# Kernel tuning notes

Measured on AMD Instinct MI355X. Metric: run time of the kernel, lower is better.

The kernel has to match this reference:

```python
import jax, jax.numpy as jnp
import numpy as np

L = 3        # num_layers
B = 8192     # batch slots
H = 1024     # hidden_dim (== decoder_in_dim)
D_IN = 1024
D_OUT = 80
N_ACT = 4096 # active rows selected by hidden_idx


def setup_inputs() -> dict:
    key = jax.random.key(0)
    ks = jax.random.split(key, 8)
    encoded = jax.random.normal(ks[0], (B, D_IN), jnp.float32)
    hidden = jax.random.normal(ks[1], (L, B, H), jnp.float32)
    hidden_idx = jnp.arange(N_ACT, dtype=jnp.int32)  # unique, in-range batch indices
    s = 0.05  # small init scale for stable gate math
    w_ih = jax.random.normal(ks[2], (L, 3 * H, D_IN), jnp.float32) * s
    w_hh = jax.random.normal(ks[3], (L, 3 * H, H), jnp.float32) * s
    b_ih = jax.random.normal(ks[4], (L, 3 * H), jnp.float32) * s
    b_hh = jax.random.normal(ks[5], (L, 3 * H), jnp.float32) * s
    w_out = jax.random.normal(ks[6], (D_OUT, H), jnp.float32) * s
    b_out = jax.random.normal(ks[7], (D_OUT,), jnp.float32) * s
    return {"encoded": encoded, "hidden": hidden, "hidden_idx": hidden_idx,
            "w_ih": w_ih, "w_hh": w_hh, "b_ih": b_ih, "b_hh": b_hh,
            "w_out": w_out, "b_out": b_out}


def reference(encoded, hidden, hidden_idx, w_ih, w_hh, b_ih, b_hh, w_out, b_out):
    # Gather active rows, run stacked GRUCells, scatter back (eval mode: dropout = identity).
    x = encoded[hidden_idx]                       # [N, D_IN]
    new_hidden = []
    for i in range(L):                            # small fixed layer loop
        h_full = hidden[i]                        # [B, H]
        h = h_full[hidden_idx]                    # [N, H]
        gi = x @ w_ih[i].T + b_ih[i]              # [N, 3H] gates from input
        gh = h @ w_hh[i].T + b_hh[i]              # [N, 3H] gates from hidden
        i_r, i_z, i_n = jnp.split(gi, 3, axis=-1)
        h_r, h_z, h_n = jnp.split(gh, 3, axis=-1)
        r = jax.nn.sigmoid(i_r + h_r)
        z = jax.nn.sigmoid(i_z + h_z)
        n = jnp.tanh(i_n + r * h_n)
        h_out = (1.0 - z) * n + z * h             # torch GRUCell update
        x = h_out
        new_hidden.append(h_full.at[hidden_idx].set(h_out))
    y = jnp.tanh(x @ w_out.T + b_out)             # linear head + tanh activation
    output = jnp.zeros((B, D_OUT), y.dtype).at[hidden_idx].set(y)
    return (output, jnp.stack(new_hidden))
```

## Files before the change

kernel.cpp:

```cpp
#include <hip/hip_runtime.h>

typedef unsigned short ushort_t;
typedef unsigned int uint_t;
typedef __attribute__((ext_vector_type(8))) short bf16x8;
typedef __attribute__((ext_vector_type(4))) float f32x4;

constexpr int L_   = 3;
constexpr int B_   = 8192;
constexpr int H_   = 1024;
constexpr int DIN_ = 1024;
constexpr int DOUT_= 80;
constexpr int NACT_= 4096;
constexpr int G3_  = 3 * H_;

static __device__ __forceinline__ ushort_t f2bf(float f) {
    uint_t u = __float_as_uint(f);
    uint_t r = (u + 0x7FFFu + ((u >> 16) & 1u)) >> 16;
    return (ushort_t)r;
}

static __device__ __forceinline__ void gll16(const void* g, void* l) {
    __builtin_amdgcn_global_load_lds(
        (const __attribute__((address_space(1))) uint32_t*)g,
        (__attribute__((address_space(3))) uint32_t*)l, 16, 0, 0);
}

__global__ void prep_convert(const float* __restrict__ wih, const float* __restrict__ whh,
                             const float* __restrict__ wout,
                             ushort_t* __restrict__ oih, ushort_t* __restrict__ ohh,
                             ushort_t* __restrict__ oout) {
    int tid = blockIdx.x * blockDim.x + threadIdx.x;
    int nth = gridDim.x * blockDim.x;
    const int NW = L_ * G3_ * H_ / 4;
    for (int i = tid; i < NW; i += nth) {
        float4 a = ((const float4*)wih)[i];
        ushort4 o; o.x = f2bf(a.x); o.y = f2bf(a.y); o.z = f2bf(a.z); o.w = f2bf(a.w);
        ((ushort4*)oih)[i] = o;
        float4 b = ((const float4*)whh)[i];
        ushort4 p; p.x = f2bf(b.x); p.y = f2bf(b.y); p.z = f2bf(b.z); p.w = f2bf(b.w);
        ((ushort4*)ohh)[i] = p;
    }
    const int NO = DOUT_ * H_ / 4;
    for (int i = tid; i < NO; i += nth) {
        float4 a = ((const float4*)wout)[i];
        ushort4 o; o.x = f2bf(a.x); o.y = f2bf(a.y); o.z = f2bf(a.z); o.w = f2bf(a.w);
        ((ushort4*)oout)[i] = o;
    }
}

__global__ void prep_gather(const float* __restrict__ encoded, const float* __restrict__ hidden,
                            const int* __restrict__ idx,
                            ushort_t* __restrict__ x0, ushort_t* __restrict__ hb) {
    const int C4 = H_ / 4;
    const int PER = NACT_ * C4;
    int tid = blockIdx.x * blockDim.x + threadIdx.x;
    int nth = gridDim.x * blockDim.x;
    int total = 4 * PER;
    for (int i = tid; i < total; i += nth) {
        int seg = i / PER;
        int rem = i - seg * PER;
        int r = rem / C4, c = rem % C4;
        int gr = idx[r];
        const float* src = (seg == 0) ? (encoded + (size_t)gr * DIN_)
                                      : (hidden + ((size_t)(seg - 1) * B_ + gr) * H_);
        float4 v = ((const float4*)src)[c];
        ushort4 o; o.x = f2bf(v.x); o.y = f2bf(v.y); o.z = f2bf(v.z); o.w = f2bf(v.w);
        ushort_t* dst = (seg == 0) ? x0 : (hb + (size_t)(seg - 1) * NACT_ * H_);
        ((ushort4*)(dst + (size_t)r * H_))[c] = o;
    }
}

__global__ __launch_bounds__(256, 2) void gru_layer(
    const ushort_t* __restrict__ xb,
    const ushort_t* __restrict__ hb,
    const float* __restrict__ hid_full,
    const ushort_t* __restrict__ wih,
    const ushort_t* __restrict__ whh,
    const float* __restrict__ bih, const float* __restrict__ bhh,
    const int* __restrict__ idx,
    float* __restrict__ out_hid,
    ushort_t* __restrict__ xnext)
{
    __shared__ ushort_t As[128 * 64];
    __shared__ ushort_t Ws[192 * 64];

    const int tid = threadIdx.x;
    const int bid = blockIdx.x;
    const int swz = (bid & 7) * 64 + (bid >> 3);
    const int bn = swz & 15, bm = swz >> 4;
    const int row0 = bm * 128, col0 = bn * 64;
    const int wave = tid >> 6, lane = tid & 63;
    const int wr = wave >> 1, wc = wave & 1;
    const int fl = lane & 15, fh = lane >> 4;
    const int srow = lane >> 3;
    const int sxor = ((lane & 7) ^ srow) * 8;

    f32x4 accR[4][2] = {};
    f32x4 accZ[4][2] = {};
    f32x4 accN[2][4][2] = {};

#pragma unroll
    for (int ph = 0; ph < 2; ++ph) {
        const ushort_t* Asrc = ph ? hb : xb;
        const ushort_t* Wsrc = ph ? whh : wih;
        const ushort_t* abase[4];
        const ushort_t* wbase[6];
#pragma unroll
        for (int t = 0; t < 4; ++t)
            abase[t] = Asrc + (size_t)(row0 + wave * 32 + t * 8 + srow) * H_ + sxor;
#pragma unroll
        for (int t = 0; t < 6; ++t) {
            const int slot = wave * 48 + t * 8 + srow;
            const int gate = slot >> 6, rowW = slot & 63;
            wbase[t] = Wsrc + (size_t)(gate * H_ + col0 + rowW) * H_ + sxor;
        }
        for (int kk = 0; kk < H_; kk += 64) {
            __syncthreads();
#pragma unroll
            for (int t = 0; t < 4; ++t)
                gll16(abase[t] + kk, &As[wave * 2048 + t * 512]);
#pragma unroll
            for (int t = 0; t < 6; ++t)
                gll16(wbase[t] + kk, &Ws[wave * 3072 + t * 512]);
            __syncthreads();
#pragma unroll
            for (int ks = 0; ks < 2; ++ks) {
                const int sl = ((ks * 4 + fh) ^ (fl & 7)) * 8;
                bf16x8 a[4];
#pragma unroll
                for (int m = 0; m < 4; ++m)
                    a[m] = *(const bf16x8*)&As[(wr * 64 + m * 16 + fl) * 64 + sl];
#pragma unroll
                for (int g = 0; g < 3; ++g) {
#pragma unroll
                    for (int n = 0; n < 2; ++n) {
                        const bf16x8 b = *(const bf16x8*)&Ws[(g * 64 + wc * 32 + n * 16 + fl) * 64 + sl];
#pragma unroll
                        for (int m = 0; m < 4; ++m) {
                            if (g == 0)
                                accR[m][n] = __builtin_amdgcn_mfma_f32_16x16x32_bf16(a[m], b, accR[m][n], 0, 0, 0);
                            else if (g == 1)
                                accZ[m][n] = __builtin_amdgcn_mfma_f32_16x16x32_bf16(a[m], b, accZ[m][n], 0, 0, 0);
                            else
                                accN[ph][m][n] = __builtin_amdgcn_mfma_f32_16x16x32_bf16(a[m], b, accN[ph][m][n], 0, 0, 0);
                        }
                    }
                }
            }
        }
    }

#pragma unroll
    for (int m = 0; m < 4; ++m) {
#pragma unroll
        for (int n = 0; n < 2; ++n) {
            const int c = col0 + wc * 32 + n * 16 + fl;
            const float br_r = bih[c] + bhh[c];
            const float br_z = bih[H_ + c] + bhh[H_ + c];
            const float bi_n = bih[2 * H_ + c];
            const float bh_n = bhh[2 * H_ + c];
#pragma unroll
            for (int j = 0; j < 4; ++j) {
                const int r = row0 + wr * 64 + m * 16 + fh * 4 + j;
                const float vr = 1.f / (1.f + expf(-(accR[m][n][j] + br_r)));
                const float vz = 1.f / (1.f + expf(-(accZ[m][n][j] + br_z)));
                const float vn = tanhf(accN[0][m][n][j] + bi_n + vr * (accN[1][m][n][j] + bh_n));
                const int gr = idx[r];
                const float h0 = hid_full[(size_t)gr * H_ + c];
                const float ho = (1.f - vz) * vn + vz * h0;
                out_hid[(size_t)gr * H_ + c] = ho;
                xnext[(size_t)r * H_ + c] = f2bf(ho);
            }
        }
    }
}

__global__ __launch_bounds__(256) void head_gemm(
    const ushort_t* __restrict__ xb, const ushort_t* __restrict__ wo,
    const float* __restrict__ bo, const int* __restrict__ idx,
    float* __restrict__ outy)
{
    __shared__ ushort_t Xs[64][72];
    __shared__ ushort_t Ws[80][72];
    const int tid = threadIdx.x;
    const int row0 = blockIdx.x * 64;
    const int lrow = tid >> 2, lseg = tid & 3;
    const int wave = tid >> 6, lane = tid & 63;
    const int fl = lane & 15, fh = lane >> 4;
    f32x4 acc[5] = {};

    for (int kk = 0; kk < H_; kk += 64) {
        __syncthreads();
        const ushort_t* xp = xb + (size_t)(row0 + lrow) * H_ + kk + lseg * 16;
        *(uint4*)&Xs[lrow][lseg * 16]     = *(const uint4*)xp;
        *(uint4*)&Xs[lrow][lseg * 16 + 8] = *(const uint4*)(xp + 8);
        for (int t = tid; t < 320; t += 256) {
            int r = t >> 2, s = t & 3;
            const ushort_t* wp = wo + (size_t)r * H_ + kk + s * 16;
            *(uint4*)&Ws[r][s * 16]     = *(const uint4*)wp;
            *(uint4*)&Ws[r][s * 16 + 8] = *(const uint4*)(wp + 8);
        }
        __syncthreads();
#pragma unroll
        for (int ks = 0; ks < 64; ks += 32) {
            bf16x8 a = *(const bf16x8*)&Xs[wave * 16 + fl][ks + fh * 8];
#pragma unroll
            for (int nf = 0; nf < 5; ++nf) {
                bf16x8 b = *(const bf16x8*)&Ws[nf * 16 + fl][ks + fh * 8];
                acc[nf] = __builtin_amdgcn_mfma_f32_16x16x32_bf16(a, b, acc[nf], 0, 0, 0);
            }
        }
    }
#pragma unroll
    for (int nf = 0; nf < 5; ++nf) {
        const int c = nf * 16 + fl;
        const float bb = bo[c];
#pragma unroll
        for (int j = 0; j < 4; ++j) {
            const int r = row0 + wave * 16 + fh * 4 + j;
            const float y = tanhf(acc[nf][j] + bb);
            outy[(size_t)idx[r] * DOUT_ + c] = y;
        }
    }
}

extern "C" void kernel_launch(void* const* d_in, const int* in_sizes, int n_in,
                              void* d_out, int out_size, void* d_ws, size_t ws_size,
                              hipStream_t stream) {
    const float* encoded = (const float*)d_in[0];
    const float* hidden  = (const float*)d_in[1];
    const int*   idx     = (const int*)d_in[2];
    const float* w_ih    = (const float*)d_in[3];
    const float* w_hh    = (const float*)d_in[4];
    const float* b_ih    = (const float*)d_in[5];
    const float* b_hh    = (const float*)d_in[6];
    const float* w_out   = (const float*)d_in[7];
    const float* b_out   = (const float*)d_in[8];

    float* outy = (float*)d_out;
    float* outh = outy + (size_t)B_ * DOUT_;

    ushort_t* ws    = (ushort_t*)d_ws;
    ushort_t* wihb  = ws;
    ushort_t* whhb  = wihb + (size_t)L_ * G3_ * H_;
    ushort_t* woutb = whhb + (size_t)L_ * G3_ * H_;
    ushort_t* xb0   = woutb + (size_t)DOUT_ * H_;
    ushort_t* xb1   = xb0 + (size_t)NACT_ * H_;
    ushort_t* hb    = xb1 + (size_t)NACT_ * H_;

    hipMemsetAsync(outy, 0, (size_t)B_ * DOUT_ * sizeof(float), stream);
    hipMemcpyAsync(outh, hidden, (size_t)L_ * B_ * H_ * sizeof(float),
                   hipMemcpyDeviceToDevice, stream);

    prep_convert<<<2048, 256, 0, stream>>>(w_ih, w_hh, w_out, wihb, whhb, woutb);
    prep_gather<<<2048, 256, 0, stream>>>(encoded, hidden, idx, xb0, hb);

    ushort_t* xin = xb0;
    ushort_t* xout = xb1;
    for (int i = 0; i < L_; ++i) {
        gru_layer<<<512, 256, 0, stream>>>(
            xin, hb + (size_t)i * NACT_ * H_, hidden + (size_t)i * B_ * H_,
            wihb + (size_t)i * G3_ * H_, whhb + (size_t)i * G3_ * H_,
            b_ih + (size_t)i * G3_, b_hh + (size_t)i * G3_, idx,
            outh + (size_t)i * B_ * H_, xout);
        ushort_t* t = xin; xin = xout; xout = t;
    }
    head_gemm<<<64, 256, 0, stream>>>(xin, woutb, b_out, idx, outy);
}
```

Baseline: 289.1 us.

## Double-buffer GRU GEMM with 256x64 tiles and copy only inactive hidden rows

The GRU layer kernel is rebuilt with 512-thread blocks computing 256x64 tiles. It double-buffers LDS with async global-to-LDS loads, uses explicit waitcnt/barrier scheduling and setprio around MFMA clusters, and remaps blocks across XCDs. The full device-to-device copy of hidden is replaced by a mask build plus a kernel that copies only rows not selected by hidden_idx, which cuts redundant writes of rows the GRU kernel overwrites anyway. This adds extra launches and relies on hand-tuned synchronization that could be fragile.

```diff
diff --git a/kernel.cpp b/kernel.cpp
--- a/kernel.cpp
+++ b/kernel.cpp
@@ -1,6 +1,7 @@
 #include <hip/hip_runtime.h>
 
 typedef unsigned short ushort_t;
+typedef unsigned char uchar_t;
 typedef unsigned int uint_t;
 typedef __attribute__((ext_vector_type(8))) short bf16x8;
 typedef __attribute__((ext_vector_type(4))) float f32x4;
@@ -8,10 +9,10 @@
 constexpr int L_   = 3;
 constexpr int B_   = 8192;
 constexpr int H_   = 1024;
-constexpr int DIN_ = 1024;
 constexpr int DOUT_= 80;
 constexpr int NACT_= 4096;
 constexpr int G3_  = 3 * H_;
+constexpr int BUFELT = (256 + 192) * 64;
 
 static __device__ __forceinline__ ushort_t f2bf(float f) {
     uint_t u = __float_as_uint(f);
@@ -24,6 +25,10 @@
         (const __attribute__((address_space(1))) uint32_t*)g,
         (__attribute__((address_space(3))) uint32_t*)l, 16, 0, 0);
 }
+
+#define MFMA(A, B, C) __builtin_amdgcn_mfma_f32_16x16x32_bf16((A), (B), (C), 0, 0, 0)
+#define RDA(buf, m, ks) (*(const bf16x8*)&(buf)[((wr * 128 + (m) * 16 + fl) << 6) + (((((ks) * 4) + fh) ^ (fl & 7)) << 3)])
+#define RDB(buf, g, ks) (*(const bf16x8*)&(buf)[16384 + (((g) * 64 + wc * 16 + fl) << 6) + (((((ks) * 4) + fh) ^ (fl & 7)) << 3)])
 
 __global__ void prep_convert(const float* __restrict__ wih, const float* __restrict__ whh,
                              const float* __restrict__ wout,
@@ -61,7 +66,7 @@
         int rem = i - seg * PER;
         int r = rem / C4, c = rem % C4;
         int gr = idx[r];
-        const float* src = (seg == 0) ? (encoded + (size_t)gr * DIN_)
+        const float* src = (seg == 0) ? (encoded + (size_t)gr * H_)
                                       : (hidden + ((size_t)(seg - 1) * B_ + gr) * H_);
         float4 v = ((const float4*)src)[c];
         ushort4 o; o.x = f2bf(v.x); o.y = f2bf(v.y); o.z = f2bf(v.z); o.w = f2bf(v.w);
@@ -70,107 +75,135 @@
     }
 }
 
-__global__ __launch_bounds__(256, 2) void gru_layer(
-    const ushort_t* __restrict__ xb,
-    const ushort_t* __restrict__ hb,
+__global__ void mask_build(const int* __restrict__ idx, uchar_t* __restrict__ mask) {
+    int i = blockIdx.x * blockDim.x + threadIdx.x;
+    if (i < NACT_) mask[idx[i]] = 1;
+}
+
+__global__ void copy_inactive(const float* __restrict__ hidden, const uchar_t* __restrict__ mask,
+                              float* __restrict__ outh) {
+    const int total = L_ * B_ * (H_ / 4);
+    int i = blockIdx.x * blockDim.x + threadIdx.x;
+    int nth = gridDim.x * blockDim.x;
+    for (; i < total; i += nth) {
+        int row = (i >> 8) & (B_ - 1);
+        if (mask[row]) continue;
+        ((float4*)outh)[i] = ((const float4*)hidden)[i];
+    }
+}
+
+template<bool LAST>
+static __device__ __forceinline__ void gru_ph16(
+    const ushort_t* __restrict__ sA, const ushort_t* __restrict__ sW,
+    const ushort_t* __restrict__ nA, const ushort_t* __restrict__ nW,
+    const uint_t* aoff, const uint_t* woff,
+    ushort_t* ldsbuf, int wave, int wr, int wc, int fl, int fh,
+    f32x4 (&accR)[8], f32x4 (&accZ)[8], f32x4 (&accN)[8])
+{
+#pragma unroll 2
+    for (int kki = 0; kki < 16; ++kki) {
+        ushort_t* p = ldsbuf + (kki & 1) * BUFELT;
+        ushort_t* q = ldsbuf + ((kki + 1) & 1) * BUFELT;
+        if (kki < 15) {
+#pragma unroll
+            for (int t = 0; t < 4; ++t) gll16(sA + aoff[t] + (kki + 1) * 64, q + (wave * 32 + t * 8) * 64);
+#pragma unroll
+            for (int t = 0; t < 3; ++t) gll16(sW + woff[t] + (kki + 1) * 64, q + 16384 + (wave * 24 + t * 8) * 64);
+            asm volatile("s_waitcnt vmcnt(7)" ::: "memory");
+        } else if (!LAST) {
+#pragma unroll
+            for (int t = 0; t < 4; ++t) gll16(nA + aoff[t], q + (wave * 32 + t * 8) * 64);
+#pragma unroll
+            for (int t = 0; t < 3; ++t) gll16(nW + woff[t], q + 16384 + (wave * 24 + t * 8) * 64);
+            asm volatile("s_waitcnt vmcnt(7)" ::: "memory");
+        } else {
+            asm volatile("s_waitcnt vmcnt(0)" ::: "memory");
+        }
+        __builtin_amdgcn_s_barrier();
+        bf16x8 bfr[3][2];
+#pragma unroll
+        for (int pp = 0; pp < 4; ++pp) {
+            const int m0 = pp * 2, m1 = pp * 2 + 1;
+            bf16x8 a00 = RDA(p, m0, 0), a01 = RDA(p, m0, 1);
+            bf16x8 a10 = RDA(p, m1, 0), a11 = RDA(p, m1, 1);
+            if (pp == 0) {
+#pragma unroll
+                for (int g = 0; g < 3; ++g) { bfr[g][0] = RDB(p, g, 0); bfr[g][1] = RDB(p, g, 1); }
+            }
+            __builtin_amdgcn_s_barrier();
+            asm volatile("s_waitcnt lgkmcnt(0)" ::: "memory");
+            __builtin_amdgcn_sched_barrier(0);
+            __builtin_amdgcn_s_setprio(1);
+            accR[m0] = MFMA(a00, bfr[0][0], accR[m0]); accR[m0] = MFMA(a01, bfr[0][1], accR[m0]);
+            accR[m1] = MFMA(a10, bfr[0][0], accR[m1]); accR[m1] = MFMA(a11, bfr[0][1], accR[m1]);
+            accZ[m0] = MFMA(a00, bfr[1][0], accZ[m0]); accZ[m0] = MFMA(a01, bfr[1][1], accZ[m0]);
+            accZ[m1] = MFMA(a10, bfr[1][0], accZ[m1]); accZ[m1] = MFMA(a11, bfr[1][1], accZ[m1]);
+            accN[m0] = MFMA(a00, bfr[2][0], accN[m0]); accN[m0] = MFMA(a01, bfr[2][1], accN[m0]);
+            accN[m1] = MFMA(a10, bfr[2][0], accN[m1]); accN[m1] = MFMA(a11, bfr[2][1], accN[m1]);
+            __builtin_amdgcn_s_setprio(0);
+            __builtin_amdgcn_s_barrier();
+        }
+    }
+}
+
+__global__ __launch_bounds__(512, 2) void gru_layer(
+    const ushort_t* __restrict__ xb, const ushort_t* __restrict__ hb,
     const float* __restrict__ hid_full,
-    const ushort_t* __restrict__ wih,
-    const ushort_t* __restrict__ whh,
+    const ushort_t* __restrict__ wih, const ushort_t* __restrict__ whh,
     const float* __restrict__ bih, const float* __restrict__ bhh,
-    const int* __restrict__ idx,
-    float* __restrict__ out_hid,
+    const int* __restrict__ idx, float* __restrict__ out_hid,
     ushort_t* __restrict__ xnext)
 {
-    __shared__ ushort_t As[128 * 64];
-    __shared__ ushort_t Ws[192 * 64];
-
+    __shared__ ushort_t lds[2 * BUFELT];
     const int tid = threadIdx.x;
     const int bid = blockIdx.x;
-    const int swz = (bid & 7) * 64 + (bid >> 3);
-    const int bn = swz & 15, bm = swz >> 4;
-    const int row0 = bm * 128, col0 = bn * 64;
+    const int xcd = bid & 7, loc = bid >> 3;
+    const int bm = (xcd >> 1) * 4 + (loc & 3);
+    const int bn = (xcd & 1) * 8 + (loc >> 2);
+    const int row0 = bm * 256, col0 = bn * 64;
     const int wave = tid >> 6, lane = tid & 63;
-    const int wr = wave >> 1, wc = wave & 1;
+    const int wr = wave >> 2, wc = wave & 3;
     const int fl = lane & 15, fh = lane >> 4;
-    const int srow = lane >> 3;
-    const int sxor = ((lane & 7) ^ srow) * 8;
-
-    f32x4 accR[4][2] = {};
-    f32x4 accZ[4][2] = {};
-    f32x4 accN[2][4][2] = {};
-
-#pragma unroll
-    for (int ph = 0; ph < 2; ++ph) {
-        const ushort_t* Asrc = ph ? hb : xb;
-        const ushort_t* Wsrc = ph ? whh : wih;
-        const ushort_t* abase[4];
-        const ushort_t* wbase[6];
-#pragma unroll
-        for (int t = 0; t < 4; ++t)
-            abase[t] = Asrc + (size_t)(row0 + wave * 32 + t * 8 + srow) * H_ + sxor;
-#pragma unroll
-        for (int t = 0; t < 6; ++t) {
-            const int slot = wave * 48 + t * 8 + srow;
-            const int gate = slot >> 6, rowW = slot & 63;
-            wbase[t] = Wsrc + (size_t)(gate * H_ + col0 + rowW) * H_ + sxor;
-        }
-        for (int kk = 0; kk < H_; kk += 64) {
-            __syncthreads();
-#pragma unroll
-            for (int t = 0; t < 4; ++t)
-                gll16(abase[t] + kk, &As[wave * 2048 + t * 512]);
-#pragma unroll
-            for (int t = 0; t < 6; ++t)
-                gll16(wbase[t] + kk, &Ws[wave * 3072 + t * 512]);
-            __syncthreads();
-#pragma unroll
-            for (int ks = 0; ks < 2; ++ks) {
-                const int sl = ((ks * 4 + fh) ^ (fl & 7)) * 8;
-                bf16x8 a[4];
-#pragma unroll
-                for (int m = 0; m < 4; ++m)
-                    a[m] = *(const bf16x8*)&As[(wr * 64 + m * 16 + fl) * 64 + sl];
-#pragma unroll
-                for (int g = 0; g < 3; ++g) {
-#pragma unroll
-                    for (int n = 0; n < 2; ++n) {
-                        const bf16x8 b = *(const bf16x8*)&Ws[(g * 64 + wc * 32 + n * 16 + fl) * 64 + sl];
-#pragma unroll
-                        for (int m = 0; m < 4; ++m) {
-                            if (g == 0)
-                                accR[m][n] = __builtin_amdgcn_mfma_f32_16x16x32_bf16(a[m], b, accR[m][n], 0, 0, 0);
-                            else if (g == 1)
-                                accZ[m][n] = __builtin_amdgcn_mfma_f32_16x16x32_bf16(a[m], b, accZ[m][n], 0, 0, 0);
-                            else
-                                accN[ph][m][n] = __builtin_amdgcn_mfma_f32_16x16x32_bf16(a[m], b, accN[ph][m][n], 0, 0, 0);
-                        }
-                    }
-                }
-            }
-        }
-    }
-
-#pragma unroll
-    for (int m = 0; m < 4; ++m) {
-#pragma unroll
-        for (int n = 0; n < 2; ++n) {
-            const int c = col0 + wc * 32 + n * 16 + fl;
-            const float br_r = bih[c] + bhh[c];
-            const float br_z = bih[H_ + c] + bhh[H_ + c];
-            const float bi_n = bih[2 * H_ + c];
-            const float bh_n = bhh[2 * H_ + c];
-#pragma unroll
-            for (int j = 0; j < 4; ++j) {
-                const int r = row0 + wr * 64 + m * 16 + fh * 4 + j;
-                const float vr = 1.f / (1.f + expf(-(accR[m][n][j] + br_r)));
-                const float vz = 1.f / (1.f + expf(-(accZ[m][n][j] + br_z)));
-                const float vn = tanhf(accN[0][m][n][j] + bi_n + vr * (accN[1][m][n][j] + bh_n));
-                const int gr = idx[r];
-                const float h0 = hid_full[(size_t)gr * H_ + c];
-                const float ho = (1.f - vz) * vn + vz * h0;
-                out_hid[(size_t)gr * H_ + c] = ho;
-                xnext[(size_t)r * H_ + c] = f2bf(ho);
-            }
+    const int sr = lane >> 3, ss = (lane & 7) ^ sr;
+
+    uint_t aoff[4], woff[3];
+#pragma unroll
+    for (int t = 0; t < 4; ++t)
+        aoff[t] = (uint_t)(row0 + wave * 32 + t * 8 + sr) * H_ + ss * 8;
+#pragma unroll
+    for (int t = 0; t < 3; ++t) {
+        int r = wave * 24 + t * 8 + sr;
+        woff[t] = (uint_t)((r >> 6) * H_ + col0 + (r & 63)) * H_ + ss * 8;
+    }
+
+    f32x4 accR[8] = {}, accZ[8] = {}, accNx[8] = {}, accNh[8] = {};
+
+#pragma unroll
+    for (int t = 0; t < 4; ++t) gll16(xb + aoff[t], lds + (wave * 32 + t * 8) * 64);
+#pragma unroll
+    for (int t = 0; t < 3; ++t) gll16(wih + woff[t], lds + 16384 + (wave * 24 + t * 8) * 64);
+
+    gru_ph16<false>(xb, wih, hb, whh, aoff, woff, lds, wave, wr, wc, fl, fh, accR, accZ, accNx);
+    gru_ph16<true >(hb, whh, nullptr, nullptr, aoff, woff, lds, wave, wr, wc, fl, fh, accR, accZ, accNh);
+
+    const int c = col0 + wc * 16 + fl;
+    const float br_r = bih[c] + bhh[c];
+    const float br_z = bih[H_ + c] + bhh[H_ + c];
+    const float bi_n = bih[2 * H_ + c];
+    const float bh_n = bhh[2 * H_ + c];
+#pragma unroll
+    for (int m = 0; m < 8; ++m) {
+#pragma unroll
+        for (int j = 0; j < 4; ++j) {
+            const int r = row0 + wr * 128 + m * 16 + fh * 4 + j;
+            const float vr = 1.f / (1.f + expf(-(accR[m][j] + br_r)));
+            const float vz = 1.f / (1.f + expf(-(accZ[m][j] + br_z)));
+            const float vn = tanhf(accNx[m][j] + bi_n + vr * (accNh[m][j] + bh_n));
+            const int gr = idx[r];
+            const float h0 = hid_full[(size_t)gr * H_ + c];
+            const float ho = (1.f - vz) * vn + vz * h0;
+            out_hid[(size_t)gr * H_ + c] = ho;
+            xnext[(size_t)r * H_ + c] = f2bf(ho);
         }
     }
 }
@@ -247,18 +280,18 @@
     ushort_t* xb0   = woutb + (size_t)DOUT_ * H_;
     ushort_t* xb1   = xb0 + (size_t)NACT_ * H_;
     ushort_t* hb    = xb1 + (size_t)NACT_ * H_;
+    uchar_t*  mask  = (uchar_t*)(hb + (size_t)L_ * NACT_ * H_);
 
     hipMemsetAsync(outy, 0, (size_t)B_ * DOUT_ * sizeof(float), stream);
-    hipMemcpyAsync(outh, hidden, (size_t)L_ * B_ * H_ * sizeof(float),
-                   hipMemcpyDeviceToDevice, stream);
-
+    hipMemsetAsync(mask, 0, B_, stream);
+    mask_build<<<16, 256, 0, stream>>>(idx, mask);
     prep_convert<<<2048, 256, 0, stream>>>(w_ih, w_hh, w_out, wihb, whhb, woutb);
     prep_gather<<<2048, 256, 0, stream>>>(encoded, hidden, idx, xb0, hb);
 
     ushort_t* xin = xb0;
     ushort_t* xout = xb1;
     for (int i = 0; i < L_; ++i) {
-        gru_layer<<<512, 256, 0, stream>>>(
+        gru_layer<<<256, 512, 0, stream>>>(
             xin, hb + (size_t)i * NACT_ * H_, hidden + (size_t)i * B_ * H_,
             wihb + (size_t)i * G3_ * H_, whhb + (size_t)i * G3_ * H_,
             b_ih + (size_t)i * G3_, b_hh + (size_t)i * G3_, idx,
@@ -266,4 +299,5 @@
         ushort_t* t = xin; xin = xout; xout = t;
     }
     head_gemm<<<64, 256, 0, stream>>>(xin, woutb, b_out, idx, outy);
-}
+    copy_inactive<<<2048, 256, 0, stream>>>(hidden, mask, outh);
+}
```

New measurement: 295.9 us. 2.3% more time.
